# Kernel optimization log

Measured on AMD Instinct MI355X. Metric: run time of the kernel, lower is better.

The kernel has to match this reference:

```python
import jax, jax.numpy as jnp
import numpy as np

_SIZE = 9  # kernel half-width -> 19x19 kernel
_EPS = 0.0001

def _gaussian_kernel(size: int, mean: float, std: float) -> jnp.ndarray:
    t = jnp.arange(-size, size + 1, dtype=jnp.float32)
    # Normal(mean, std) pdf
    vals = jnp.exp(-0.5 * ((t - mean) / std) ** 2) / (std * np.sqrt(2.0 * np.pi))
    k2d = jnp.outer(vals, vals)
    return k2d / jnp.sum(k2d)

def _blur(x, k):
    # x: [B,H,W,3], k: [19,19]; depthwise conv, SAME padding, same kernel per channel
    kern = jnp.tile(k[:, :, None, None], (1, 1, 1, 3))  # HWIO with I=1, O=3 (grouped)
    return jax.lax.conv_general_dilated(
        x, kern, window_strides=(1, 1), padding='SAME',
        dimension_numbers=('NHWC', 'HWIO', 'NHWC'), feature_group_count=3)

def setup_inputs() -> dict:
    key = jax.random.key(0)
    k1, k2 = jax.random.split(key)
    x0 = jax.random.uniform(k1, (32, 512, 512, 3), dtype=jnp.float32)
    mask = jnp.ones((32, 512, 512, 1), dtype=jnp.float32)
    return {"x0": x0, "mask": mask}

def reference(x0, mask):
    k = _gaussian_kernel(_SIZE, 0.0, 1.0)
    mean = _blur(x0, k)                      # local mean per channel
    centered = x0 - mean
    var = _blur(centered ** 2, k)            # local variance per channel
    std = jnp.sqrt(var) + _EPS
    out = (centered / std) * mask            # mask broadcasts over channel dim
    # Original concatenates in order [red, blue, green] where split gives
    # channels (0,1,2) named (red, blue, green) -> output channel order == input order.
    return out
```

## Files before the change

### kernel.cpp

```cpp
#include <hip/hip_runtime.h>
#include <math.h>


#define TW 32
#define TH 64
#define S1W 132
#define S1R 48
#define B2R 74
#define NT  512

__global__ __launch_bounds__(NT, 4)
void lecun_lcn_kernel(const float* __restrict__ x,
                      const float* __restrict__ mask,
                      float* __restrict__ out)
{
    __shared__ float s1h[S1R * S1W];
    __shared__ float b2[B2R * S1W];

    const int tid = threadIdx.x;
    const int w0  = blockIdx.x * TW;
    const int h0  = blockIdx.y * TH;
    const int bi  = blockIdx.z;
    const int fc0 = 3 * w0 - 15;

    const float K[6] = {
        3.9894227826685783e-01f,
        2.4197072322439816e-01f,
        5.3990966224238430e-02f,
        4.4318483882270000e-03f,
        1.3383022504889000e-04f,
        1.4867195067806000e-06f
    };

    const float* xb = x + (size_t)bi * 512 * 1536;

    auto p1_task = [&](int ss, int slot, int run) {
        const int h = h0 - 10 + ss;
        float* dst = &s1h[slot * S1W + run * 16];
        if ((unsigned)h >= 512u) {
            float4 z = make_float4(0.f, 0.f, 0.f, 0.f);
            ((float4*)dst)[0] = z; ((float4*)dst)[1] = z;
            ((float4*)dst)[2] = z; ((float4*)dst)[3] = z;
            return;
        }
        const float* xrow = xb + (size_t)h * 1536;
        const int gc0 = fc0 + run * 16;
        const int a   = gc0 - 17;
        float w[48];
        if (a >= 0 && a <= 1536 - 48) {
            const float4* p = (const float4*)(xrow + a);
            #pragma unroll
            for (int q = 0; q < 12; ++q) {
                float4 v = p[q];
                w[4*q+0] = v.x; w[4*q+1] = v.y; w[4*q+2] = v.z; w[4*q+3] = v.w;
            }
        } else {
            #pragma unroll
            for (int i = 0; i < 48; ++i) {
                int j = a + i;
                w[i] = ((unsigned)j < 1536u) ? xrow[j] : 0.0f;
            }
        }
        float v1[16];
        #pragma unroll
        for (int i = 0; i < 16; ++i) {
            const int ci = 17 + i;
            float acc = K[0] * w[ci];
            #pragma unroll
            for (int d = 1; d <= 5; ++d)
                acc = fmaf(K[d], w[ci - 3*d] + w[ci + 3*d], acc);
            v1[i] = acc;
        }
        ((float4*)dst)[0] = make_float4(v1[0],  v1[1],  v1[2],  v1[3]);
        ((float4*)dst)[1] = make_float4(v1[4],  v1[5],  v1[6],  v1[7]);
        ((float4*)dst)[2] = make_float4(v1[8],  v1[9],  v1[10], v1[11]);
        ((float4*)dst)[3] = make_float4(v1[12], v1[13], v1[14], v1[15]);
    };

    auto p2_run = [&](int rb, int cnt) {
        const int quad = tid & 31;
        const int c4   = quad * 4;
        const int gcb  = fc0 + c4;
        const bool cv0 = (unsigned)(gcb + 0) < 1536u;
        const bool cv1 = (unsigned)(gcb + 1) < 1536u;
        const bool cv2 = (unsigned)(gcb + 2) < 1536u;
        const bool cv3 = (unsigned)(gcb + 3) < 1536u;
        float4 w[13];
        #pragma unroll
        for (int k = 0; k < 13; ++k) {
            if (k < cnt + 10) {
                const int ss = rb + k;
                const int sl = (ss >= S1R) ? ss - S1R : ss;
                w[k] = *(const float4*)&s1h[sl * S1W + c4];
            }
        }
        #pragma unroll
        for (int j = 0; j < 3; ++j) {
            if (j < cnt) {
                const int br = rb + j;
                const int h = h0 - 5 + br;
                float4* dst = (float4*)&b2[br * S1W + c4];
                if ((unsigned)h >= 512u) {
                    *dst = make_float4(0.f, 0.f, 0.f, 0.f);
                } else {
                    float m0 = K[0] * w[j+5].x, m1 = K[0] * w[j+5].y;
                    float m2 = K[0] * w[j+5].z, m3 = K[0] * w[j+5].w;
                    #pragma unroll
                    for (int d = 1; d <= 5; ++d) {
                        float4 aa = w[j + 5 - d];
                        float4 bb = w[j + 5 + d];
                        m0 = fmaf(K[d], aa.x + bb.x, m0);
                        m1 = fmaf(K[d], aa.y + bb.y, m1);
                        m2 = fmaf(K[d], aa.z + bb.z, m2);
                        m3 = fmaf(K[d], aa.w + bb.w, m3);
                    }
                    const float* xrow = xb + (size_t)h * 1536;
                    float c0 = cv0 ? (xrow[gcb + 0] - m0) : 0.0f;
                    float c1 = cv1 ? (xrow[gcb + 1] - m1) : 0.0f;
                    float c2 = cv2 ? (xrow[gcb + 2] - m2) : 0.0f;
                    float c3 = cv3 ? (xrow[gcb + 3] - m3) : 0.0f;
                    *dst = make_float4(c0, c1, c2, c3);
                }
            }
        }
    };

    float* vc = s1h;
    auto p3_half = [&](int vbase) {
        const int quad = tid & 31;
        const int rt   = tid >> 5;
        const int c4   = quad * 4;
        const int v0   = vbase + 2 * rt;
        float4 w[12];
        #pragma unroll
        for (int k = 0; k < 12; ++k) {
            float4 t = *(const float4*)&b2[(v0 + k) * S1W + c4];
            w[k] = make_float4(t.x*t.x, t.y*t.y, t.z*t.z, t.w*t.w);
        }
        #pragma unroll
        for (int j = 0; j < 2; ++j) {
            float s0 = K[0] * w[j+5].x, s1v = K[0] * w[j+5].y;
            float s2v = K[0] * w[j+5].z, s3 = K[0] * w[j+5].w;
            #pragma unroll
            for (int d = 1; d <= 5; ++d) {
                float4 aa = w[j + 5 - d];
                float4 bb = w[j + 5 + d];
                s0  = fmaf(K[d], aa.x + bb.x, s0);
                s1v = fmaf(K[d], aa.y + bb.y, s1v);
                s2v = fmaf(K[d], aa.z + bb.z, s2v);
                s3  = fmaf(K[d], aa.w + bb.w, s3);
            }
            *(float4*)&vc[(v0 - vbase + j) * S1W + c4] =
                make_float4(s0, s1v, s2v, s3);
        }
    };

    auto p4_half = [&](int rbase) {
        if (tid >= 256) return;
        const int r    = rbase + (tid >> 3);
        const int run  = tid & 7;
        const int tc0  = run * 12;
        float w[44];
        #pragma unroll
        for (int q = 0; q < 11; ++q) {
            float4 v = *(const float4*)&vc[(r - rbase) * S1W + tc0 + 4*q];
            w[4*q+0] = v.x; w[4*q+1] = v.y; w[4*q+2] = v.z; w[4*q+3] = v.w;
        }
        float cw[16];
        #pragma unroll
        for (int q = 0; q < 4; ++q) {
            float4 v = *(const float4*)&b2[(r + 5) * S1W + tc0 + 12 + 4*q];
            cw[4*q+0] = v.x; cw[4*q+1] = v.y; cw[4*q+2] = v.z; cw[4*q+3] = v.w;
        }
        const int h = h0 + r;
        const size_t rowoff = (size_t)(bi * 512 + h);
        const float* mrow = mask + rowoff * 512 + w0 + 4 * run;
        float mv[4];
        #pragma unroll
        for (int k = 0; k < 4; ++k) mv[k] = mrow[k];
        float o[12];
        #pragma unroll
        for (int j = 0; j < 12; ++j) {
            const int ci = 15 + j;
            float var = K[0] * w[ci];
            #pragma unroll
            for (int d = 1; d <= 5; ++d)
                var = fmaf(K[d], w[ci - 3*d] + w[ci + 3*d], var);
            o[j] = cw[j + 3] * __builtin_amdgcn_rcpf(sqrtf(var) + 1e-4f) * mv[j / 3];
        }
        float* orow = &out[rowoff * 1536 + 3 * w0 + tc0];
        ((float4*)orow)[0] = make_float4(o[0], o[1], o[2],  o[3]);
        ((float4*)orow)[1] = make_float4(o[4], o[5], o[6],  o[7]);
        ((float4*)orow)[2] = make_float4(o[8], o[9], o[10], o[11]);
    };

    if (tid < 384) p1_task(tid >> 3, tid >> 3, tid & 7);
    __syncthreads();

    {
        const int rt  = tid >> 5;
        const int cnt = (rt < 6) ? 3 : 2;
        const int rb  = (rt < 6) ? 3 * rt : 18 + 2 * (rt - 6);
        p2_run(rb, cnt);
    }
    __syncthreads();

    if (tid < 288) p1_task(48 + (tid >> 3), tid >> 3, tid & 7);
    __syncthreads();

    {
        const int rt  = tid >> 5;
        const int cnt = (rt < 4) ? 3 : 2;
        const int rb  = (rt < 4) ? 38 + 3 * rt : 50 + 2 * (rt - 4);
        p2_run(rb, cnt);
    }
    __syncthreads();

    p3_half(0);
    __syncthreads();
    p4_half(0);
    __syncthreads();
    p3_half(32);
    __syncthreads();
    p4_half(32);
}

extern "C" void kernel_launch(void* const* d_in, const int* in_sizes, int n_in,
                              void* d_out, int out_size, void* d_ws, size_t ws_size,
                              hipStream_t stream) {
    const float* x0   = (const float*)d_in[0];
    const float* mask = (const float*)d_in[1];
    float* out = (float*)d_out;

    dim3 grid(512 / TW, 512 / TH, 32);
    dim3 block(NT);
    lecun_lcn_kernel<<<grid, block, 0, stream>>>(x0, mask, out);
}
```

Measured before the change: 309.9 us.

## Make variance phases wave-local to drop block-wide barriers

Replaces the final vertical-variance and horizontal-variance/output phases, which were split into halves separated by three block barriers, with a per-wavefront scheme. Each wave computes 4 rows of vertical variance into its own shared-memory scratch slice and immediately consumes them, using only an LDS wait instead of __syncthreads. This is meant to cut barrier stalls and let waves progress independently. In exchange, only half of each wave's lanes run the output stage, and correctness relies on intra-wave ordering of shared-memory writes and reads.

```diff
diff --git a/kernel.cpp b/kernel.cpp
--- a/kernel.cpp
+++ b/kernel.cpp
@@ -125,75 +125,6 @@
         }
     };
 
-    float* vc = s1h;
-    auto p3_half = [&](int vbase) {
-        const int quad = tid & 31;
-        const int rt   = tid >> 5;
-        const int c4   = quad * 4;
-        const int v0   = vbase + 2 * rt;
-        float4 w[12];
-        #pragma unroll
-        for (int k = 0; k < 12; ++k) {
-            float4 t = *(const float4*)&b2[(v0 + k) * S1W + c4];
-            w[k] = make_float4(t.x*t.x, t.y*t.y, t.z*t.z, t.w*t.w);
-        }
-        #pragma unroll
-        for (int j = 0; j < 2; ++j) {
-            float s0 = K[0] * w[j+5].x, s1v = K[0] * w[j+5].y;
-            float s2v = K[0] * w[j+5].z, s3 = K[0] * w[j+5].w;
-            #pragma unroll
-            for (int d = 1; d <= 5; ++d) {
-                float4 aa = w[j + 5 - d];
-                float4 bb = w[j + 5 + d];
-                s0  = fmaf(K[d], aa.x + bb.x, s0);
-                s1v = fmaf(K[d], aa.y + bb.y, s1v);
-                s2v = fmaf(K[d], aa.z + bb.z, s2v);
-                s3  = fmaf(K[d], aa.w + bb.w, s3);
-            }
-            *(float4*)&vc[(v0 - vbase + j) * S1W + c4] =
-                make_float4(s0, s1v, s2v, s3);
-        }
-    };
-
-    auto p4_half = [&](int rbase) {
-        if (tid >= 256) return;
-        const int r    = rbase + (tid >> 3);
-        const int run  = tid & 7;
-        const int tc0  = run * 12;
-        float w[44];
-        #pragma unroll
-        for (int q = 0; q < 11; ++q) {
-            float4 v = *(const float4*)&vc[(r - rbase) * S1W + tc0 + 4*q];
-            w[4*q+0] = v.x; w[4*q+1] = v.y; w[4*q+2] = v.z; w[4*q+3] = v.w;
-        }
-        float cw[16];
-        #pragma unroll
-        for (int q = 0; q < 4; ++q) {
-            float4 v = *(const float4*)&b2[(r + 5) * S1W + tc0 + 12 + 4*q];
-            cw[4*q+0] = v.x; cw[4*q+1] = v.y; cw[4*q+2] = v.z; cw[4*q+3] = v.w;
-        }
-        const int h = h0 + r;
-        const size_t rowoff = (size_t)(bi * 512 + h);
-        const float* mrow = mask + rowoff * 512 + w0 + 4 * run;
-        float mv[4];
-        #pragma unroll
-        for (int k = 0; k < 4; ++k) mv[k] = mrow[k];
-        float o[12];
-        #pragma unroll
-        for (int j = 0; j < 12; ++j) {
-            const int ci = 15 + j;
-            float var = K[0] * w[ci];
-            #pragma unroll
-            for (int d = 1; d <= 5; ++d)
-                var = fmaf(K[d], w[ci - 3*d] + w[ci + 3*d], var);
-            o[j] = cw[j + 3] * __builtin_amdgcn_rcpf(sqrtf(var) + 1e-4f) * mv[j / 3];
-        }
-        float* orow = &out[rowoff * 1536 + 3 * w0 + tc0];
-        ((float4*)orow)[0] = make_float4(o[0], o[1], o[2],  o[3]);
-        ((float4*)orow)[1] = make_float4(o[4], o[5], o[6],  o[7]);
-        ((float4*)orow)[2] = make_float4(o[8], o[9], o[10], o[11]);
-    };
-
     if (tid < 384) p1_task(tid >> 3, tid >> 3, tid & 7);
     __syncthreads();
 
@@ -216,13 +147,81 @@
     }
     __syncthreads();
 
-    p3_half(0);
-    __syncthreads();
-    p4_half(0);
-    __syncthreads();
-    p3_half(32);
-    __syncthreads();
-    p4_half(32);
+    {
+        const int wv   = tid >> 6;
+        const int lane = tid & 63;
+        float* vscr = &s1h[(wv * 4) * S1W];
+        const int q   = lane & 31;
+        const int hf  = lane >> 5;
+        const int c4  = q * 4;
+        const int rr  = (lane >> 3) & 3;
+        const int run = lane & 7;
+        const int tc0 = run * 12;
+
+        #pragma unroll
+        for (int ck = 0; ck < 2; ++ck) {
+            const int r0 = wv * 8 + ck * 4;
+            {
+                float4 w[12];
+                #pragma unroll
+                for (int k = 0; k < 12; ++k) {
+                    float4 t = *(const float4*)&b2[(r0 + 2*hf + k) * S1W + c4];
+                    w[k] = make_float4(t.x*t.x, t.y*t.y, t.z*t.z, t.w*t.w);
+                }
+                #pragma unroll
+                for (int j2 = 0; j2 < 2; ++j2) {
+                    float s0  = K[0]*w[j2+5].x, s1v = K[0]*w[j2+5].y;
+                    float s2v = K[0]*w[j2+5].z, s3  = K[0]*w[j2+5].w;
+                    #pragma unroll
+                    for (int d = 1; d <= 5; ++d) {
+                        float4 aa = w[j2+5-d], bb = w[j2+5+d];
+                        s0  = fmaf(K[d], aa.x+bb.x, s0);
+                        s1v = fmaf(K[d], aa.y+bb.y, s1v);
+                        s2v = fmaf(K[d], aa.z+bb.z, s2v);
+                        s3  = fmaf(K[d], aa.w+bb.w, s3);
+                    }
+                    *(float4*)&vscr[(2*hf + j2) * S1W + c4] =
+                        make_float4(s0, s1v, s2v, s3);
+                }
+            }
+            asm volatile("s_waitcnt lgkmcnt(0)" ::: "memory");
+            if (lane < 32) {
+                float w[44];
+                #pragma unroll
+                for (int qq = 0; qq < 11; ++qq) {
+                    float4 v = *(const float4*)&vscr[rr * S1W + tc0 + 4*qq];
+                    w[4*qq+0]=v.x; w[4*qq+1]=v.y; w[4*qq+2]=v.z; w[4*qq+3]=v.w;
+                }
+                float cw[16];
+                #pragma unroll
+                for (int qq = 0; qq < 4; ++qq) {
+                    float4 v = *(const float4*)&b2[(r0 + rr + 5) * S1W + tc0 + 12 + 4*qq];
+                    cw[4*qq+0]=v.x; cw[4*qq+1]=v.y; cw[4*qq+2]=v.z; cw[4*qq+3]=v.w;
+                }
+                const int h = h0 + r0 + rr;
+                const size_t rowoff = (size_t)(bi * 512 + h);
+                const float* mrow = mask + rowoff * 512 + w0 + 4 * run;
+                float mv[4];
+                #pragma unroll
+                for (int k2 = 0; k2 < 4; ++k2) mv[k2] = mrow[k2];
+                float o[12];
+                #pragma unroll
+                for (int j = 0; j < 12; ++j) {
+                    const int ci = 15 + j;
+                    float var = K[0] * w[ci];
+                    #pragma unroll
+                    for (int d = 1; d <= 5; ++d)
+                        var = fmaf(K[d], w[ci - 3*d] + w[ci + 3*d], var);
+                    o[j] = cw[j + 3] * __builtin_amdgcn_rcpf(sqrtf(var) + 1e-4f) * mv[j / 3];
+                }
+                float* orow = &out[rowoff * 1536 + 3 * w0 + tc0];
+                ((float4*)orow)[0] = make_float4(o[0], o[1], o[2],  o[3]);
+                ((float4*)orow)[1] = make_float4(o[4], o[5], o[6],  o[7]);
+                ((float4*)orow)[2] = make_float4(o[8], o[9], o[10], o[11]);
+            }
+            asm volatile("" ::: "memory");
+        }
+    }
 }
 
 extern "C" void kernel_launch(void* const* d_in, const int* in_sizes, int n_in,
```

Result: slower. 316.6 us (+2.2%).

## Halve tile height, use 256-thread blocks, align halo for vectorized float4 loads

Applied to the files above, without the earlier changes.

Tile height drops from 64 to 32 rows and blocks from 512 to 256 threads, so LDS per block falls from about 64KB to about 39KB. The column halo shifts to start at 3*w0-16, which aligns it to float4 so the centered-value x reads and the mask reads become single float4 loads. The two-half variance and normalize passes merge into one pass each, removing two barriers. In exchange, the relative halo recompute grows (52 first-pass rows per 32 output rows, against 84 per 64), but more, smaller blocks can be resident at once.

```diff
diff --git a/kernel.cpp b/kernel.cpp
--- a/kernel.cpp
+++ b/kernel.cpp
@@ -3,11 +3,11 @@
 
 
 #define TW 32
-#define TH 64
+#define TH 32
 #define S1W 132
-#define S1R 48
-#define B2R 74
-#define NT  512
+#define S1R 32
+#define B2R 42
+#define NT  256
 
 __global__ __launch_bounds__(NT, 4)
 void lecun_lcn_kernel(const float* __restrict__ x,
@@ -21,7 +21,7 @@
     const int w0  = blockIdx.x * TW;
     const int h0  = blockIdx.y * TH;
     const int bi  = blockIdx.z;
-    const int fc0 = 3 * w0 - 15;
+    const int fc0 = 3 * w0 - 16;
 
     const float K[6] = {
         3.9894227826685783e-01f,
@@ -45,7 +45,7 @@
         }
         const float* xrow = xb + (size_t)h * 1536;
         const int gc0 = fc0 + run * 16;
-        const int a   = gc0 - 17;
+        const int a   = gc0 - 16;
         float w[48];
         if (a >= 0 && a <= 1536 - 48) {
             const float4* p = (const float4*)(xrow + a);
@@ -64,7 +64,7 @@
         float v1[16];
         #pragma unroll
         for (int i = 0; i < 16; ++i) {
-            const int ci = 17 + i;
+            const int ci = 16 + i;
             float acc = K[0] * w[ci];
             #pragma unroll
             for (int d = 1; d <= 5; ++d)
@@ -78,21 +78,15 @@
     };
 
     auto p2_run = [&](int rb, int cnt) {
-        const int quad = tid & 31;
-        const int c4   = quad * 4;
-        const int gcb  = fc0 + c4;
-        const bool cv0 = (unsigned)(gcb + 0) < 1536u;
-        const bool cv1 = (unsigned)(gcb + 1) < 1536u;
-        const bool cv2 = (unsigned)(gcb + 2) < 1536u;
-        const bool cv3 = (unsigned)(gcb + 3) < 1536u;
+        const int q   = tid & 31;
+        const int c4  = q * 4;
+        const int gcb = fc0 + c4;
+        const bool cvAll = (gcb >= 0) && (gcb <= 1536 - 4);
         float4 w[13];
         #pragma unroll
         for (int k = 0; k < 13; ++k) {
-            if (k < cnt + 10) {
-                const int ss = rb + k;
-                const int sl = (ss >= S1R) ? ss - S1R : ss;
-                w[k] = *(const float4*)&s1h[sl * S1W + c4];
-            }
+            if (k < cnt + 10)
+                w[k] = *(const float4*)&s1h[((rb + k) & 31) * S1W + c4];
         }
         #pragma unroll
         for (int j = 0; j < 3; ++j) {
@@ -100,7 +94,7 @@
                 const int br = rb + j;
                 const int h = h0 - 5 + br;
                 float4* dst = (float4*)&b2[br * S1W + c4];
-                if ((unsigned)h >= 512u) {
+                if ((unsigned)h >= 512u || !cvAll) {
                     *dst = make_float4(0.f, 0.f, 0.f, 0.f);
                 } else {
                     float m0 = K[0] * w[j+5].x, m1 = K[0] * w[j+5].y;
@@ -115,30 +109,50 @@
                         m3 = fmaf(K[d], aa.w + bb.w, m3);
                     }
                     const float* xrow = xb + (size_t)h * 1536;
-                    float c0 = cv0 ? (xrow[gcb + 0] - m0) : 0.0f;
-                    float c1 = cv1 ? (xrow[gcb + 1] - m1) : 0.0f;
-                    float c2 = cv2 ? (xrow[gcb + 2] - m2) : 0.0f;
-                    float c3 = cv3 ? (xrow[gcb + 3] - m3) : 0.0f;
-                    *dst = make_float4(c0, c1, c2, c3);
+                    float4 xv = *(const float4*)(xrow + gcb);
+                    *dst = make_float4(xv.x - m0, xv.y - m1,
+                                       xv.z - m2, xv.w - m3);
                 }
             }
         }
     };
 
+    p1_task(tid >> 3, tid >> 3, tid & 7);
+    __syncthreads();
+
+    {
+        const int rt  = tid >> 5;
+        const int cnt = (rt < 6) ? 3 : 2;
+        const int rb  = (rt < 6) ? 3 * rt : 18 + 2 * (rt - 6);
+        p2_run(rb, cnt);
+    }
+    __syncthreads();
+
+    if (tid < 160) p1_task(32 + (tid >> 3), tid >> 3, tid & 7);
+    __syncthreads();
+
+    {
+        const int rt  = tid >> 5;
+        const int cnt = (rt < 4) ? 3 : 2;
+        const int rb  = (rt < 4) ? 22 + 3 * rt : 34 + 2 * (rt - 4);
+        p2_run(rb, cnt);
+    }
+    __syncthreads();
+
     float* vc = s1h;
-    auto p3_half = [&](int vbase) {
-        const int quad = tid & 31;
-        const int rt   = tid >> 5;
-        const int c4   = quad * 4;
-        const int v0   = vbase + 2 * rt;
-        float4 w[12];
-        #pragma unroll
-        for (int k = 0; k < 12; ++k) {
-            float4 t = *(const float4*)&b2[(v0 + k) * S1W + c4];
+    {
+        const int q  = tid & 31;
+        const int rt = tid >> 5;
+        const int r0 = rt * 4;
+        const int c4 = q * 4;
+        float4 w[14];
+        #pragma unroll
+        for (int k = 0; k < 14; ++k) {
+            float4 t = *(const float4*)&b2[(r0 + k) * S1W + c4];
             w[k] = make_float4(t.x*t.x, t.y*t.y, t.z*t.z, t.w*t.w);
         }
         #pragma unroll
-        for (int j = 0; j < 2; ++j) {
+        for (int j = 0; j < 4; ++j) {
             float s0 = K[0] * w[j+5].x, s1v = K[0] * w[j+5].y;
             float s2v = K[0] * w[j+5].z, s3 = K[0] * w[j+5].w;
             #pragma unroll
@@ -150,79 +164,46 @@
                 s2v = fmaf(K[d], aa.z + bb.z, s2v);
                 s3  = fmaf(K[d], aa.w + bb.w, s3);
             }
-            *(float4*)&vc[(v0 - vbase + j) * S1W + c4] =
-                make_float4(s0, s1v, s2v, s3);
-        }
-    };
-
-    auto p4_half = [&](int rbase) {
-        if (tid >= 256) return;
-        const int r    = rbase + (tid >> 3);
+            *(float4*)&vc[(r0 + j) * S1W + c4] = make_float4(s0, s1v, s2v, s3);
+        }
+    }
+    __syncthreads();
+
+    {
+        const int r    = tid >> 3;
         const int run  = tid & 7;
         const int tc0  = run * 12;
         float w[44];
         #pragma unroll
-        for (int q = 0; q < 11; ++q) {
-            float4 v = *(const float4*)&vc[(r - rbase) * S1W + tc0 + 4*q];
-            w[4*q+0] = v.x; w[4*q+1] = v.y; w[4*q+2] = v.z; w[4*q+3] = v.w;
-        }
-        float cw[16];
-        #pragma unroll
-        for (int q = 0; q < 4; ++q) {
-            float4 v = *(const float4*)&b2[(r + 5) * S1W + tc0 + 12 + 4*q];
-            cw[4*q+0] = v.x; cw[4*q+1] = v.y; cw[4*q+2] = v.z; cw[4*q+3] = v.w;
+        for (int qq = 0; qq < 11; ++qq) {
+            float4 v = *(const float4*)&vc[r * S1W + tc0 + 4*qq];
+            w[4*qq+0] = v.x; w[4*qq+1] = v.y; w[4*qq+2] = v.z; w[4*qq+3] = v.w;
+        }
+        float cw[12];
+        #pragma unroll
+        for (int qq = 0; qq < 3; ++qq) {
+            float4 v = *(const float4*)&b2[(r + 5) * S1W + tc0 + 16 + 4*qq];
+            cw[4*qq+0] = v.x; cw[4*qq+1] = v.y; cw[4*qq+2] = v.z; cw[4*qq+3] = v.w;
         }
         const int h = h0 + r;
         const size_t rowoff = (size_t)(bi * 512 + h);
-        const float* mrow = mask + rowoff * 512 + w0 + 4 * run;
-        float mv[4];
-        #pragma unroll
-        for (int k = 0; k < 4; ++k) mv[k] = mrow[k];
+        float4 mv4 = *(const float4*)(mask + rowoff * 512 + w0 + 4 * run);
+        float mv[4] = { mv4.x, mv4.y, mv4.z, mv4.w };
         float o[12];
         #pragma unroll
         for (int j = 0; j < 12; ++j) {
-            const int ci = 15 + j;
+            const int ci = 16 + j;
             float var = K[0] * w[ci];
             #pragma unroll
             for (int d = 1; d <= 5; ++d)
                 var = fmaf(K[d], w[ci - 3*d] + w[ci + 3*d], var);
-            o[j] = cw[j + 3] * __builtin_amdgcn_rcpf(sqrtf(var) + 1e-4f) * mv[j / 3];
+            o[j] = cw[j] * __builtin_amdgcn_rcpf(sqrtf(var) + 1e-4f) * mv[j / 3];
         }
         float* orow = &out[rowoff * 1536 + 3 * w0 + tc0];
         ((float4*)orow)[0] = make_float4(o[0], o[1], o[2],  o[3]);
         ((float4*)orow)[1] = make_float4(o[4], o[5], o[6],  o[7]);
         ((float4*)orow)[2] = make_float4(o[8], o[9], o[10], o[11]);
-    };
-
-    if (tid < 384) p1_task(tid >> 3, tid >> 3, tid & 7);
-    __syncthreads();
-
-    {
-        const int rt  = tid >> 5;
-        const int cnt = (rt < 6) ? 3 : 2;
-        const int rb  = (rt < 6) ? 3 * rt : 18 + 2 * (rt - 6);
-        p2_run(rb, cnt);
-    }
-    __syncthreads();
-
-    if (tid < 288) p1_task(48 + (tid >> 3), tid >> 3, tid & 7);
-    __syncthreads();
-
-    {
-        const int rt  = tid >> 5;
-        const int cnt = (rt < 4) ? 3 : 2;
-        const int rb  = (rt < 4) ? 38 + 3 * rt : 50 + 2 * (rt - 4);
-        p2_run(rb, cnt);
-    }
-    __syncthreads();
-
-    p3_half(0);
-    __syncthreads();
-    p4_half(0);
-    __syncthreads();
-    p3_half(32);
-    __syncthreads();
-    p4_half(32);
+    }
 }
 
 extern "C" void kernel_launch(void* const* d_in, const int* in_sizes, int n_in,
```

New measurement: 279.5 us. -9.8%, faster.
